# Kernel tuning notes

Hardware: AMD Instinct MI355X
Metric: run time of the kernel (lower is better)

The kernel has to match this reference:

```python
import jax, jax.numpy as jnp
import numpy as np

N = 20000
E = 640000
H = 128
N_LAYERS = 3


def setup_inputs() -> dict:
    key = jax.random.key(0)
    ks = jax.random.split(key, 16)
    s = lambda fan_in: 1.0 / np.sqrt(fan_in)
    inp = {
        "x": jax.random.normal(ks[0], (N, 1), jnp.float32),
        "edge_index": jax.random.randint(ks[1], (2, E), 0, N, jnp.int64),
        "edge_attr": jax.random.uniform(ks[2], (E, 1), jnp.float32),
        # encoder_bfs: Linear(1, H)
        "enc_w": jax.random.uniform(ks[3], (1, H), jnp.float32, -1.0, 1.0),
        "enc_b": jax.random.uniform(ks[4], (H,), jnp.float32, -1.0, 1.0),
        # msg_net: Linear(2H+1, H)
        "msg_w": jax.random.uniform(ks[5], (2 * H + 1, H), jnp.float32, -s(2 * H + 1), s(2 * H + 1)),
        "msg_b": jax.random.uniform(ks[6], (H,), jnp.float32, -s(2 * H + 1), s(2 * H + 1)),
        # update_net: Linear(2H, H)
        "upd_w": jax.random.uniform(ks[7], (2 * H, H), jnp.float32, -s(2 * H), s(2 * H)),
        "upd_b": jax.random.uniform(ks[8], (H,), jnp.float32, -s(2 * H), s(2 * H)),
        # decoder_bfs: Linear(H, 1)
        "dec_w": jax.random.uniform(ks[9], (H, 1), jnp.float32, -s(H), s(H)),
        "dec_b": jax.random.uniform(ks[10], (1,), jnp.float32, -s(H), s(H)),
        # termination_bfs: Linear(H, 1) + Sigmoid
        "term_w": jax.random.uniform(ks[11], (H, 1), jnp.float32, -s(H), s(H)),
        "term_b": jax.random.uniform(ks[12], (1,), jnp.float32, -s(H), s(H)),
    }
    return inp


def reference(x, edge_index, edge_attr, enc_w, enc_b, msg_w, msg_b, upd_w, upd_b,
              dec_w, dec_b, term_w, term_b):
    # BFS branch of AlgorithmExecutor.forward
    h = x @ enc_w + enc_b                                  # [N, H] encoder
    src = edge_index[0]                                    # j (source)
    dst = edge_index[1]                                    # i (target)
    n = h.shape[0]
    for _ in range(N_LAYERS):
        # message: cat([x_i, x_j, edge_attr]) -> Linear -> ReLU
        combined = jnp.concatenate([h[dst], h[src], edge_attr], axis=-1)  # [E, 2H+1]
        msg = jax.nn.relu(combined @ msg_w + msg_b)                        # [E, H]
        # aggr='max': scatter-max into destination nodes; PyG zero-inits the
        # output buffer so empty nodes get 0 (messages are ReLU'd, >= 0)
        aggr = jax.ops.segment_max(msg, dst, num_segments=n)
        aggr = jnp.maximum(aggr, 0.0)
        # update: cat([x, aggr]) -> Linear -> ReLU
        h = jax.nn.relu(jnp.concatenate([h, aggr], axis=-1) @ upd_w + upd_b)
    out = jax.nn.sigmoid(h @ dec_w + dec_b)                            # [N, 1]
    term = jax.nn.sigmoid(jnp.mean(h, axis=0, keepdims=True) @ term_w + term_b)  # [1, 1]
    return out, term
```

## Files before the change

kernel.cpp:

```cpp
#include <hip/hip_runtime.h>
#include <math.h>

#define NN 20000
#define NE 640000
#define HD 128
#define ROWS 32
#define NBLK (NN / ROWS)
#define LROWS 16
#define LNBLK (NN / LROWS)
#define CAP 96

typedef __attribute__((ext_vector_type(8))) short bf16x8;
typedef __attribute__((ext_vector_type(4))) float f32x4;

__device__ __forceinline__ unsigned short f2bf(float f) {
    unsigned u = __float_as_uint(f);
    unsigned r = u + 0x7FFFu + ((u >> 16) & 1u);
    return (unsigned short)(r >> 16);
}
__device__ __forceinline__ float bf2f(unsigned short b) {
    return __uint_as_float(((unsigned)b) << 16);
}

__device__ __forceinline__ unsigned pack_edge(int src, float ea) {
    return ((unsigned)src << 17) | (unsigned)(ea * 131072.0f);
}

__global__ __launch_bounds__(256) void k_pack_fill(const float* __restrict__ msg_w,
                                                   const float* __restrict__ upd_w,
                                                   unsigned short* __restrict__ wp,
                                                   int* __restrict__ cnt) {
    int tid = blockIdx.x * 256 + threadIdx.x;
    if (tid < 8192) {
        int m = tid >> 11;
        int rem = tid & 2047;
        int ct = rem >> 8;
        int ks = (rem >> 6) & 3;
        int lane = rem & 63;
        const float* W = (m == 0) ? msg_w
                       : (m == 1) ? msg_w + HD * HD
                       : (m == 2) ? upd_w
                                  : upd_w + HD * HD;
        int k0 = ks * 32 + (lane >> 4) * 8;
        int col = ct * 16 + (lane & 15);
        unsigned short* outp = wp + (size_t)m * 16384 + ((ct * 4 + ks) * 64 + lane) * 8;
#pragma unroll
        for (int j = 0; j < 8; j++) outp[j] = f2bf(W[(k0 + j) * HD + col]);
    }
    int z = tid - 8192;
    if (z >= 0 && z < NN) cnt[z] = 0;
}

__global__ __launch_bounds__(256) void k_scatter(const int4* __restrict__ src4,
                                                 const int4* __restrict__ dst4,
                                                 const float4* __restrict__ ea4,
                                                 int* __restrict__ cnt,
                                                 unsigned* __restrict__ edges) {
    for (int e4 = blockIdx.x * 256 + threadIdx.x; e4 < NE / 4; e4 += gridDim.x * 256) {
        int4 d = dst4[e4];
        int4 s = src4[e4];
        float4 a = ea4[e4];
        int p;
        p = atomicAdd(&cnt[d.x], 1);
        if (p < CAP) edges[(size_t)d.x * CAP + p] = pack_edge(s.x, a.x);
        p = atomicAdd(&cnt[d.y], 1);
        if (p < CAP) edges[(size_t)d.y * CAP + p] = pack_edge(s.y, a.y);
        p = atomicAdd(&cnt[d.z], 1);
        if (p < CAP) edges[(size_t)d.z * CAP + p] = pack_edge(s.z, a.z);
        p = atomicAdd(&cnt[d.w], 1);
        if (p < CAP) edges[(size_t)d.w * CAP + p] = pack_edge(s.w, a.w);
    }
}

__device__ __forceinline__ bf16x8 ldfragA(const unsigned short S[][HD], int row, int ks, int q) {
    int k0 = (ks * 32 + q * 8) ^ ((row & 7) << 3);
    return *(const bf16x8*)&S[row][k0];
}

__global__ __launch_bounds__(128) void k_enc_mm1(const float* __restrict__ x,
                                                 const float* __restrict__ enc_w,
                                                 const float* __restrict__ enc_b,
                                                 const unsigned short* __restrict__ wp,
                                                 const float* __restrict__ msg_b,
                                                 unsigned short* __restrict__ h_bf,
                                                 unsigned short* __restrict__ Abf,
                                                 unsigned short* __restrict__ Bbf,
                                                 const int* __restrict__ cnt,
                                                 unsigned* __restrict__ edges) {
    __shared__ unsigned short hsN[ROWS][HD];
    int t = threadIdx.x;
    int n0 = blockIdx.x * ROWS;
    if (t < ROWS) {
        int i = n0 + t;
        int ci = cnt[i];
        if (ci > CAP) ci = CAP;
        if (ci > 0) {
            int ce = (ci + 15) & ~15;
            if (ce > CAP) ce = CAP;
            unsigned e0 = edges[(size_t)i * CAP];
            for (int j = ci; j < ce; j++) edges[(size_t)i * CAP + j] = e0;
        }
    }
    {
        float ew = enc_w[t], eb = enc_b[t];
#pragma unroll
        for (int r = 0; r < ROWS; r++) {
            unsigned short bv = f2bf(fmaf(x[n0 + r], ew, eb));
            hsN[r][t ^ ((r & 7) << 3)] = bv;
            h_bf[(size_t)(n0 + r) * HD + t] = bv;
        }
    }
    __syncthreads();
    int lane = t & 63, wv = t >> 6;
    int rbase = wv * 16;
    int cl = lane & 15, q = lane >> 4;
    const unsigned short* wd = wp;
    const unsigned short* wsr = wp + 16384;
    f32x4 aacc[8], bacc[8];
#pragma unroll
    for (int ct = 0; ct < 8; ct++) {
        float bv = msg_b[ct * 16 + cl];
        aacc[ct] = (f32x4){bv, bv, bv, bv};
        bacc[ct] = (f32x4){0.f, 0.f, 0.f, 0.f};
    }
#pragma unroll
    for (int ks = 0; ks < 4; ks++) {
        bf16x8 hF = ldfragA(hsN, rbase + cl, ks, q);
#pragma unroll
        for (int ct = 0; ct < 8; ct++) {
            bf16x8 w1 = *(const bf16x8*)&wd[((ct * 4 + ks) * 64 + lane) * 8];
            bf16x8 w2 = *(const bf16x8*)&wsr[((ct * 4 + ks) * 64 + lane) * 8];
            aacc[ct] = __builtin_amdgcn_mfma_f32_16x16x32_bf16(hF, w1, aacc[ct], 0, 0, 0);
            bacc[ct] = __builtin_amdgcn_mfma_f32_16x16x32_bf16(hF, w2, bacc[ct], 0, 0, 0);
        }
    }
#pragma unroll
    for (int ct = 0; ct < 8; ct++) {
        int col = ct * 16 + cl;
#pragma unroll
        for (int reg = 0; reg < 4; reg++) {
            int row = n0 + rbase + q * 4 + reg;
            Abf[(size_t)row * HD + col] = f2bf(aacc[ct][reg]);
            Bbf[(size_t)row * HD + col] = f2bf(bacc[ct][reg]);
        }
    }
}

template <int FINAL>
__global__ __launch_bounds__(512) void k_layer(unsigned short* __restrict__ h_bf,
                                               const unsigned short* __restrict__ Ain,
                                               const unsigned short* __restrict__ Bin,
                                               const int* __restrict__ cnt,
                                               const unsigned* __restrict__ edges,
                                               const float* __restrict__ msg_w,
                                               const unsigned short* __restrict__ wp,
                                               const float* __restrict__ upd_b,
                                               const float* __restrict__ msg_b,
                                               unsigned short* __restrict__ Aout,
                                               unsigned short* __restrict__ Bout,
                                               const float* __restrict__ dec_w,
                                               const float* __restrict__ dec_b,
                                               const float* __restrict__ term_w,
                                               float* __restrict__ out,
                                               float* __restrict__ partials) {
    __shared__ unsigned short hsA[LROWS][HD];
    __shared__ unsigned short hsG[LROWS][HD];
    __shared__ unsigned short hsN[LROWS][HD];
    __shared__ float tred[8];
    int t = threadIdx.x;
    int wv = t >> 6, lane = t & 63;
    int n0 = blockIdx.x * LROWS;

    bf16x8 hpre;
    if (t < LROWS * 16) {
        int row = t >> 4, ch = t & 15;
        hpre = *(const bf16x8*)&h_bf[(size_t)(n0 + row) * HD + ch * 8];
    }

    int i0 = n0 + wv * 2;
    int ci0 = cnt[i0], ci1 = cnt[i0 + 1];
    if (ci0 > CAP) ci0 = CAP;
    if (ci1 > CAP) ci1 = CAP;
    unsigned av0 = ((const unsigned*)Ain)[(size_t)i0 * 64 + lane];
    unsigned av1 = ((const unsigned*)Ain)[(size_t)(i0 + 1) * 64 + lane];

    float2 w = ((const float2*)(msg_w + 256 * HD))[lane];
    const float SC = 1.0f / 131072.0f;
    const unsigned* B32 = (const unsigned*)Bin;
#pragma unroll
    for (int k = 0; k < 2; k++) {
        int i = i0 + k;
        int ci = k ? ci1 : ci0;
        unsigned av = k ? av1 : av0;
        const unsigned* ep = edges + (size_t)i * CAP;
        float m0 = -INFINITY, m1 = -INFINITY;
        int nb = (ci + 15) >> 4;
        uint4 P[4];
        if (nb > 0) {
#pragma unroll
            for (int v = 0; v < 4; v++) P[v] = *(const uint4*)&ep[v * 4];
        }
        for (int bi = 0; bi < nb; bi++) {
            unsigned p[16], b[16];
#pragma unroll
            for (int v = 0; v < 4; v++) *(uint4*)&p[v * 4] = P[v];
            if (bi + 1 < nb) {
#pragma unroll
                for (int v = 0; v < 4; v++)
                    P[v] = *(const uint4*)&ep[(bi + 1) * 16 + v * 4];
            }
#pragma unroll
            for (int u = 0; u < 16; u++)
                b[u] = B32[(size_t)(p[u] >> 17) * 64 + lane];
#pragma unroll
            for (int u = 0; u < 16; u++) {
                float ea = (float)(p[u] & 0x1FFFF) * SC;
                m0 = fmaxf(m0, fmaf(ea, w.x, bf2f((unsigned short)b[u])));
                m1 = fmaxf(m1, fmaf(ea, w.y, bf2f((unsigned short)(b[u] >> 16))));
            }
        }
        unsigned short r0 = f2bf(fmaxf(bf2f((unsigned short)av) + m0, 0.f));
        unsigned short r1 = f2bf(fmaxf(bf2f((unsigned short)(av >> 16)) + m1, 0.f));
        int ri = wv * 2 + k;
        int e0 = (2 * lane) ^ ((ri & 7) << 3);
        *(unsigned*)&hsG[ri][e0] = ((unsigned)r1 << 16) | r0;
    }
    if (t < LROWS * 16) {
        int row = t >> 4, ch = t & 15;
        *(bf16x8*)&hsA[row][(ch ^ (row & 7)) * 8] = hpre;
    }
    __syncthreads();

    int q = lane >> 4, cl = lane & 15;
    int ct = wv;
    const unsigned short* wd = wp;
    const unsigned short* wsr = wp + 16384;
    const unsigned short* wu1 = wp + 2 * 16384;
    const unsigned short* wu2 = wp + 3 * 16384;
    f32x4 acc;
    {
        float bv = upd_b[ct * 16 + cl];
        acc = (f32x4){bv, bv, bv, bv};
    }
#pragma unroll
    for (int ks = 0; ks < 4; ks++) {
        bf16x8 hF = ldfragA(hsA, cl, ks, q);
        bf16x8 gF = ldfragA(hsG, cl, ks, q);
        bf16x8 w1 = *(const bf16x8*)&wu1[((ct * 4 + ks) * 64 + lane) * 8];
        bf16x8 w2 = *(const bf16x8*)&wu2[((ct * 4 + ks) * 64 + lane) * 8];
        acc = __builtin_amdgcn_mfma_f32_16x16x32_bf16(hF, w1, acc, 0, 0, 0);
        acc = __builtin_amdgcn_mfma_f32_16x16x32_bf16(gF, w2, acc, 0, 0, 0);
    }
    {
        int col = ct * 16 + cl;
#pragma unroll
        for (int reg = 0; reg < 4; reg++) {
            int row = q * 4 + reg;
            hsN[row][col ^ ((row & 7) << 3)] = f2bf(fmaxf(acc[reg], 0.f));
        }
    }
    __syncthreads();

    if (FINAL == 0) {
        f32x4 aacc, bacc;
        {
            float bv = msg_b[ct * 16 + cl];
            aacc = (f32x4){bv, bv, bv, bv};
            bacc = (f32x4){0.f, 0.f, 0.f, 0.f};
        }
#pragma unroll
        for (int ks = 0; ks < 4; ks++) {
            bf16x8 hF2 = ldfragA(hsN, cl, ks, q);
            bf16x8 w1 = *(const bf16x8*)&wd[((ct * 4 + ks) * 64 + lane) * 8];
            bf16x8 w2 = *(const bf16x8*)&wsr[((ct * 4 + ks) * 64 + lane) * 8];
            aacc = __builtin_amdgcn_mfma_f32_16x16x32_bf16(hF2, w1, aacc, 0, 0, 0);
            bacc = __builtin_amdgcn_mfma_f32_16x16x32_bf16(hF2, w2, bacc, 0, 0, 0);
        }
        {
            int col = ct * 16 + cl;
#pragma unroll
            for (int reg = 0; reg < 4; reg++) {
                int row = n0 + q * 4 + reg;
                Aout[(size_t)row * HD + col] = f2bf(aacc[reg]);
                Bout[(size_t)row * HD + col] = f2bf(bacc[reg]);
            }
        }
        __syncthreads();
        if (t < LROWS * 16) {
            int row = t >> 4, ch = t & 15;
            *(bf16x8*)&h_bf[(size_t)(n0 + row) * HD + ch * 8] =
                *(const bf16x8*)&hsN[row][(ch ^ (row & 7)) * 8];
        }
    } else {
        float dw0 = dec_w[lane], dw1 = dec_w[64 + lane];
        float tw0 = term_w[lane], tw1 = term_w[64 + lane];
        float tsum = 0.f;
#pragma unroll
        for (int rr = 0; rr < 2; rr++) {
            int r = wv * 2 + rr;
            int sw = (r & 7) << 3;
            float h0 = bf2f(hsN[r][lane ^ sw]);
            float h1 = bf2f(hsN[r][(64 + lane) ^ sw]);
            float s1 = fmaf(h0, dw0, h1 * dw1);
            float s2 = fmaf(h0, tw0, h1 * tw1);
#pragma unroll
            for (int off = 32; off; off >>= 1) {
                s1 += __shfl_xor(s1, off);
                s2 += __shfl_xor(s2, off);
            }
            if (lane == 0) out[n0 + r] = 1.f / (1.f + expf(-(s1 + dec_b[0])));
            tsum += s2;
        }
        if (lane == 0) tred[wv] = tsum;
        __syncthreads();
        if (t == 0) {
            float s = 0.f;
#pragma unroll
            for (int i = 0; i < 8; i++) s += tred[i];
            partials[blockIdx.x] = s;
        }
    }
}

__global__ __launch_bounds__(256) void k_term(const float* __restrict__ partials,
                                              const float* __restrict__ term_b,
                                              float* __restrict__ out) {
    __shared__ float red[256];
    int t = threadIdx.x;
    float s = 0.f;
    for (int i = t; i < LNBLK; i += 256) s += partials[i];
    red[t] = s;
    __syncthreads();
    for (int off = 128; off; off >>= 1) {
        if (t < off) red[t] += red[t + off];
        __syncthreads();
    }
    if (t == 0) {
        float m = red[0] / (float)NN;
        out[NN] = 1.f / (1.f + expf(-(m + term_b[0])));
    }
}

extern "C" void kernel_launch(void* const* d_in, const int* in_sizes, int n_in,
                              void* d_out, int out_size, void* d_ws, size_t ws_size,
                              hipStream_t stream) {
    const float* x        = (const float*)d_in[0];
    const int*   eidx     = (const int*)d_in[1];
    const float* eattr    = (const float*)d_in[2];
    const float* enc_w    = (const float*)d_in[3];
    const float* enc_b    = (const float*)d_in[4];
    const float* msg_w    = (const float*)d_in[5];
    const float* msg_b    = (const float*)d_in[6];
    const float* upd_w    = (const float*)d_in[7];
    const float* upd_b    = (const float*)d_in[8];
    const float* dec_w    = (const float*)d_in[9];
    const float* dec_b    = (const float*)d_in[10];
    const float* term_w   = (const float*)d_in[11];
    const float* term_b   = (const float*)d_in[12];
    float* out = (float*)d_out;

    const int* src = eidx;
    const int* dst = eidx + NE;

    char* ws = (char*)d_ws;
    size_t off = 0;
    auto alloc = [&](size_t bytes) -> void* {
        void* p = ws + off;
        off += (bytes + 255) & ~size_t(255);
        return p;
    };
    unsigned short* h_bf  = (unsigned short*)alloc((size_t)NN * HD * 2);
    unsigned short* A0    = (unsigned short*)alloc((size_t)NN * HD * 2);
    unsigned short* B0    = (unsigned short*)alloc((size_t)NN * HD * 2);
    unsigned short* A1    = (unsigned short*)alloc((size_t)NN * HD * 2);
    unsigned short* B1    = (unsigned short*)alloc((size_t)NN * HD * 2);
    unsigned* edges       = (unsigned*)alloc((size_t)NN * CAP * 4);
    unsigned short* wpack = (unsigned short*)alloc((size_t)4 * 16384 * 2);
    int*   cnt            = (int*)alloc((size_t)NN * 4);
    float* partials       = (float*)alloc((size_t)LNBLK * 4);

    k_pack_fill<<<(8192 + NN + 255) / 256, 256, 0, stream>>>(msg_w, upd_w, wpack, cnt);
    k_scatter<<<1024, 256, 0, stream>>>((const int4*)src, (const int4*)dst,
                                        (const float4*)eattr, cnt, edges);
    k_enc_mm1<<<NBLK, 128, 0, stream>>>(x, enc_w, enc_b, wpack, msg_b, h_bf, A0, B0,
                                        cnt, edges);

    k_layer<0><<<LNBLK, 512, 0, stream>>>(h_bf, A0, B0, cnt, edges, msg_w, wpack,
                                          upd_b, msg_b, A1, B1,
                                          dec_w, dec_b, term_w, out, partials);
    k_layer<0><<<LNBLK, 512, 0, stream>>>(h_bf, A1, B1, cnt, edges, msg_w, wpack,
                                          upd_b, msg_b, A0, B0,
                                          dec_w, dec_b, term_w, out, partials);
    k_layer<1><<<LNBLK, 512, 0, stream>>>(h_bf, A0, B0, cnt, edges, msg_w, wpack,
                                          upd_b, msg_b, A1, B1,
                                          dec_w, dec_b, term_w, out, partials);

    k_term<<<1, 256, 0, stream>>>(partials, term_b, out);
}
```

Before: 144.6 us.

## Partition edge scatter by destination range and stage edge lists in LDS

```diff
diff --git a/kernel.cpp b/kernel.cpp
--- a/kernel.cpp
+++ b/kernel.cpp
@@ -9,6 +9,8 @@
 #define LROWS 16
 #define LNBLK (NN / LROWS)
 #define CAP 96
+#define NPART 8
+#define PART_SZ (NN / NPART)
 
 typedef __attribute__((ext_vector_type(8))) short bf16x8;
 typedef __attribute__((ext_vector_type(4))) float f32x4;
@@ -51,24 +53,34 @@
     if (z >= 0 && z < NN) cnt[z] = 0;
 }
 
-__global__ __launch_bounds__(256) void k_scatter(const int4* __restrict__ src4,
+__global__ __launch_bounds__(256) void k_scatter(const int* __restrict__ src,
                                                  const int4* __restrict__ dst4,
-                                                 const float4* __restrict__ ea4,
+                                                 const float* __restrict__ ea,
                                                  int* __restrict__ cnt,
                                                  unsigned* __restrict__ edges) {
-    for (int e4 = blockIdx.x * 256 + threadIdx.x; e4 < NE / 4; e4 += gridDim.x * 256) {
+    int part = blockIdx.x & (NPART - 1);
+    int blk = blockIdx.x >> 3;
+    int nblk = gridDim.x >> 3;
+    int lo = part * PART_SZ;
+    for (int e4 = blk * 256 + threadIdx.x; e4 < NE / 4; e4 += nblk * 256) {
         int4 d = dst4[e4];
-        int4 s = src4[e4];
-        float4 a = ea4[e4];
-        int p;
-        p = atomicAdd(&cnt[d.x], 1);
-        if (p < CAP) edges[(size_t)d.x * CAP + p] = pack_edge(s.x, a.x);
-        p = atomicAdd(&cnt[d.y], 1);
-        if (p < CAP) edges[(size_t)d.y * CAP + p] = pack_edge(s.y, a.y);
-        p = atomicAdd(&cnt[d.z], 1);
-        if (p < CAP) edges[(size_t)d.z * CAP + p] = pack_edge(s.z, a.z);
-        p = atomicAdd(&cnt[d.w], 1);
-        if (p < CAP) edges[(size_t)d.w * CAP + p] = pack_edge(s.w, a.w);
+        int e = e4 * 4;
+        if ((unsigned)(d.x - lo) < (unsigned)PART_SZ) {
+            int p = atomicAdd(&cnt[d.x], 1);
+            if (p < CAP) edges[(size_t)d.x * CAP + p] = pack_edge(src[e], ea[e]);
+        }
+        if ((unsigned)(d.y - lo) < (unsigned)PART_SZ) {
+            int p = atomicAdd(&cnt[d.y], 1);
+            if (p < CAP) edges[(size_t)d.y * CAP + p] = pack_edge(src[e + 1], ea[e + 1]);
+        }
+        if ((unsigned)(d.z - lo) < (unsigned)PART_SZ) {
+            int p = atomicAdd(&cnt[d.z], 1);
+            if (p < CAP) edges[(size_t)d.z * CAP + p] = pack_edge(src[e + 2], ea[e + 2]);
+        }
+        if ((unsigned)(d.w - lo) < (unsigned)PART_SZ) {
+            int p = atomicAdd(&cnt[d.w], 1);
+            if (p < CAP) edges[(size_t)d.w * CAP + p] = pack_edge(src[e + 3], ea[e + 3]);
+        }
     }
 }
 
@@ -166,6 +178,7 @@
     __shared__ unsigned short hsA[LROWS][HD];
     __shared__ unsigned short hsG[LROWS][HD];
     __shared__ unsigned short hsN[LROWS][HD];
+    __shared__ unsigned erec[LROWS * CAP];
     __shared__ float tred[8];
     int t = threadIdx.x;
     int wv = t >> 6, lane = t & 63;
@@ -175,6 +188,13 @@
     if (t < LROWS * 16) {
         int row = t >> 4, ch = t & 15;
         hpre = *(const bf16x8*)&h_bf[(size_t)(n0 + row) * HD + ch * 8];
+    }
+
+    {
+        const unsigned* eg = edges + (size_t)n0 * CAP;
+#pragma unroll
+        for (int v = 0; v < (LROWS * CAP) / 512; v++)
+            erec[t + v * 512] = eg[t + v * 512];
     }
 
     int i0 = n0 + wv * 2;
@@ -183,32 +203,23 @@
     if (ci1 > CAP) ci1 = CAP;
     unsigned av0 = ((const unsigned*)Ain)[(size_t)i0 * 64 + lane];
     unsigned av1 = ((const unsigned*)Ain)[(size_t)(i0 + 1) * 64 + lane];
+    __syncthreads();
 
     float2 w = ((const float2*)(msg_w + 256 * HD))[lane];
     const float SC = 1.0f / 131072.0f;
     const unsigned* B32 = (const unsigned*)Bin;
 #pragma unroll
     for (int k = 0; k < 2; k++) {
-        int i = i0 + k;
+        int ri = wv * 2 + k;
         int ci = k ? ci1 : ci0;
         unsigned av = k ? av1 : av0;
-        const unsigned* ep = edges + (size_t)i * CAP;
+        const unsigned* ep = &erec[ri * CAP];
         float m0 = -INFINITY, m1 = -INFINITY;
         int nb = (ci + 15) >> 4;
-        uint4 P[4];
-        if (nb > 0) {
-#pragma unroll
-            for (int v = 0; v < 4; v++) P[v] = *(const uint4*)&ep[v * 4];
-        }
         for (int bi = 0; bi < nb; bi++) {
             unsigned p[16], b[16];
 #pragma unroll
-            for (int v = 0; v < 4; v++) *(uint4*)&p[v * 4] = P[v];
-            if (bi + 1 < nb) {
-#pragma unroll
-                for (int v = 0; v < 4; v++)
-                    P[v] = *(const uint4*)&ep[(bi + 1) * 16 + v * 4];
-            }
+            for (int u = 0; u < 16; u++) p[u] = ep[bi * 16 + u];
 #pragma unroll
             for (int u = 0; u < 16; u++)
                 b[u] = B32[(size_t)(p[u] >> 17) * 64 + lane];
@@ -221,7 +232,6 @@
         }
         unsigned short r0 = f2bf(fmaxf(bf2f((unsigned short)av) + m0, 0.f));
         unsigned short r1 = f2bf(fmaxf(bf2f((unsigned short)(av >> 16)) + m1, 0.f));
-        int ri = wv * 2 + k;
         int e0 = (2 * lane) ^ ((ri & 7) << 3);
         *(unsigned*)&hsG[ri][e0] = ((unsigned)r1 << 16) | r0;
     }
@@ -380,8 +390,7 @@
     float* partials       = (float*)alloc((size_t)LNBLK * 4);
 
     k_pack_fill<<<(8192 + NN + 255) / 256, 256, 0, stream>>>(msg_w, upd_w, wpack, cnt);
-    k_scatter<<<1024, 256, 0, stream>>>((const int4*)src, (const int4*)dst,
-                                        (const float4*)eattr, cnt, edges);
+    k_scatter<<<NPART * 128, 256, 0, stream>>>(src, (const int4*)dst, eattr, cnt, edges);
     k_enc_mm1<<<NBLK, 128, 0, stream>>>(x, enc_w, enc_b, wpack, msg_b, h_bf, A0, B0,
                                         cnt, edges);
 
```

New measurement: 135.5 us, median of 2. 6.3% less time.
